# Performance work log

Measured on AMD Instinct MI355X. Metric: run time of the kernel, lower is better.

Reference implementation:

```python
import jax, jax.numpy as jnp
import numpy as np
import math

B, T, D, H, L, V = 2, 1024, 768, 12, 4, 50257
HD = D // H
ROPE_PCT = 0.5
MAX_WL = 10000.0
EPS = 1e-5


def setup_inputs() -> dict:
    key = jax.random.key(0)
    ks = jax.random.split(key, 8)
    s = 0.02
    return {
        "idx": jax.random.randint(ks[0], (B, T), 0, V, dtype=jnp.int32),
        "wte": jax.random.normal(ks[1], (V, D), jnp.float32) * s,
        "ln1_g": jnp.ones((L, D), jnp.float32),
        "ln1_b": jnp.zeros((L, D), jnp.float32),
        "Wqkv": jax.random.normal(ks[2], (L, D, 3 * D), jnp.float32) * s,
        "bqkv": jnp.zeros((L, 3 * D), jnp.float32),
        "Wo": jax.random.normal(ks[3], (L, D, D), jnp.float32) * s,
        "bo": jnp.zeros((L, D), jnp.float32),
        "ln2_g": jnp.ones((L, D), jnp.float32),
        "ln2_b": jnp.zeros((L, D), jnp.float32),
        "Wfc": jax.random.normal(ks[4], (L, D, 4 * D), jnp.float32) * s,
        "bfc": jnp.zeros((L, 4 * D), jnp.float32),
        "Wp": jax.random.normal(ks[5], (L, 4 * D, D), jnp.float32) * s,
        "bp": jnp.zeros((L, D), jnp.float32),
        "lnf_g": jnp.ones((D,), jnp.float32),
        "lnf_b": jnp.zeros((D,), jnp.float32),
        "Wlm": jax.random.normal(ks[6], (D, V), jnp.float32) * s,
    }


def _ln(x, g, b):
    m = x.mean(-1, keepdims=True)
    v = x.var(-1, keepdims=True)
    return (x - m) / jnp.sqrt(v + EPS) * g + b


def _gelu(x):
    return 0.5 * x * (1.0 + jnp.tanh(math.sqrt(2.0 / math.pi) * (x + 0.044715 * x ** 3)))


def _p_rope(x, positions):
    # x: [B, H, T, HD]; partial RoPE: rotate first ROPE_PCT of angle pairs, leave rest.
    rope_angles = int(ROPE_PCT * HD // 2)
    nope_angles = HD // 2 - rope_angles
    fraction = 2.0 * jnp.arange(0, rope_angles) / HD
    timescale = jnp.power(MAX_WL, fraction)
    timescale = jnp.pad(timescale, (0, nope_angles), constant_values=jnp.inf)
    sinusoid = positions[:, None] / timescale[None, :]  # [T, HD//2]; pos/inf = 0 -> no rotation
    sin, cos = jnp.sin(sinusoid), jnp.cos(sinusoid)
    first, second = jnp.split(x, 2, axis=-1)
    out = jnp.concatenate([first * cos - second * sin, second * cos + first * sin], axis=-1)
    return out.astype(x.dtype)


def reference(idx, wte, ln1_g, ln1_b, Wqkv, bqkv, Wo, bo, ln2_g, ln2_b, Wfc, bfc, Wp, bp, lnf_g, lnf_b, Wlm):
    x = wte[idx]  # [B, T, D]
    positions = jnp.arange(T, dtype=x.dtype)
    causal = jnp.tril(jnp.ones((T, T), dtype=bool))
    scale = jnp.sqrt(jnp.float32(HD)).astype(x.dtype)
    for l in range(L):
        h1 = _ln(x, ln1_g[l], ln1_b[l])
        h2 = _ln(x, ln2_g[l], ln2_b[l])  # note: both LNs read the same x (as in source)
        # attention
        qkv = h1 @ Wqkv[l] + bqkv[l]
        q, k, v = jnp.split(qkv, 3, axis=-1)
        sh = lambda t: t.reshape(B, T, H, HD).transpose(0, 2, 1, 3)
        q, k, v = sh(q), sh(k), sh(v)
        q = _p_rope(q, positions)
        k = _p_rope(k, positions)
        att = jnp.einsum('bhqd,bhkd->bhqk', q, k) / scale
        att = jnp.where(causal, att, jnp.finfo(att.dtype).min)
        att = jax.nn.softmax(att, axis=-1)
        y = jnp.einsum('bhqk,bhkd->bhqd', att, v)
        y = y.transpose(0, 2, 1, 3).reshape(B, T, D)
        x = x + (y @ Wo[l] + bo[l])
        # MLP
        h = _gelu(h2 @ Wfc[l] + bfc[l])
        x = x + (h @ Wp[l] + bp[l])
    x = _ln(x, lnf_g, lnf_b)
    logits = x @ Wlm  # [B, T, V]
    return logits
```

## Files before the change

### kernel.cpp

```cpp
#include <hip/hip_runtime.h>

typedef unsigned short u16;
typedef unsigned int u32;
typedef __attribute__((ext_vector_type(8))) short bf16x8;
typedef __attribute__((ext_vector_type(4))) float f32x4;

#define SEQ 1024
#define DM 768
#define NH 12
#define HD2 64
#define NLAYER 4
#define NVOCAB 50257
#define BT 2048

__device__ __forceinline__ u16 f2bf(float f) {
  union { float f; u32 u; } v; v.f = f;
  u32 r = v.u + 0x7FFFu + ((v.u >> 16) & 1u);
  return (u16)(r >> 16);
}
__device__ __forceinline__ float bf2f(u16 u) {
  union { u32 u; float f; } v; v.u = ((u32)u) << 16;
  return v.f;
}

__device__ __forceinline__ void glds16(const u16* g, u16* l) {
  __builtin_amdgcn_global_load_lds(
      (const __attribute__((address_space(1))) u32*)(const void*)g,
      (__attribute__((address_space(3))) u32*)(void*)l, 16, 0, 0);
}

__device__ __forceinline__ void cvt_tile(const float* __restrict__ in,
                                         u16* __restrict__ out, int R, int C,
                                         int cx, int ry, u16 (*t)[68]) {
  int c0 = cx * 64, r0 = ry * 64;
  int tx = threadIdx.x & 15, ty = threadIdx.x >> 4;
  int c = c0 + tx * 4;
#pragma unroll
  for (int i = 0; i < 4; ++i) {
    int r = r0 + ty + i * 16;
    float4 v = make_float4(0.f, 0.f, 0.f, 0.f);
    if (c + 3 < C) {
      v = *(const float4*)&in[(size_t)r * C + c];
    } else {
      if (c + 0 < C) v.x = in[(size_t)r * C + c];
      if (c + 1 < C) v.y = in[(size_t)r * C + c + 1];
      if (c + 2 < C) v.z = in[(size_t)r * C + c + 2];
      if (c + 3 < C) v.w = in[(size_t)r * C + c + 3];
    }
    t[ty + i * 16][tx * 4 + 0] = f2bf(v.x);
    t[ty + i * 16][tx * 4 + 1] = f2bf(v.y);
    t[ty + i * 16][tx * 4 + 2] = f2bf(v.z);
    t[ty + i * 16][tx * 4 + 3] = f2bf(v.w);
  }
  __syncthreads();
  int wl = threadIdx.x & 31, grp = threadIdx.x >> 5;
#pragma unroll
  for (int it = 0; it < 8; ++it) {
    int cc = it * 8 + grp;
    int gcol = c0 + cc;
    if (gcol < C) {
      u32 wv = (u32)t[2 * wl][cc] | ((u32)t[2 * wl + 1][cc] << 16);
      *(u32*)&out[(size_t)gcol * R + r0 + 2 * wl] = wv;
    }
  }
}

__global__ void k_prep(const int* __restrict__ idx, const float* __restrict__ wte,
                       float* __restrict__ xf, float* __restrict__ ctab,
                       float* __restrict__ stab, const float* __restrict__ Wqkv,
                       const float* __restrict__ Wo, const float* __restrict__ Wfc,
                       const float* __restrict__ Wp, const float* __restrict__ Wlm,
                       u16* __restrict__ wqkvT, u16* __restrict__ woT,
                       u16* __restrict__ wfcT, u16* __restrict__ wpT,
                       u16* __restrict__ wlmT) {
  __shared__ u16 t[64][68];
  int bid = blockIdx.x;
  if (bid < BT) {
    int tok = idx[bid];
    const float* s = wte + (size_t)tok * DM;
    float* d = xf + (size_t)bid * DM;
    for (int c = threadIdx.x; c < DM; c += 256) d[c] = s[c];
    return;
  }
  bid -= BT;
  if (bid < 64) {
    int gid = bid * 256 + threadIdx.x;
    int tt = gid >> 4, j = gid & 15;
    float inv = powf(10000.f, -(float)j * (1.f / 32.f));
    float ang = (float)tt * inv;
    ctab[gid] = cosf(ang);
    stab[gid] = sinf(ang);
    return;
  }
  bid -= 64;
  if (bid < NLAYER * 1728) {
    int layer = bid / 1728, r = bid % 1728;
    if (r < 432) {
      cvt_tile(Wqkv + (size_t)layer * DM * 3 * DM,
               wqkvT + (size_t)layer * 3 * DM * DM, DM, 3 * DM, r % 36, r / 36, t);
      return;
    }
    r -= 432;
    if (r < 144) {
      cvt_tile(Wo + (size_t)layer * DM * DM, woT + (size_t)layer * DM * DM,
               DM, DM, r % 12, r / 12, t);
      return;
    }
    r -= 144;
    if (r < 576) {
      cvt_tile(Wfc + (size_t)layer * DM * 4 * DM,
               wfcT + (size_t)layer * 4 * DM * DM, DM, 4 * DM, r % 48, r / 48, t);
      return;
    }
    r -= 576;
    cvt_tile(Wp + (size_t)layer * 4 * DM * DM, wpT + (size_t)layer * 4 * DM * DM,
             4 * DM, DM, r % 12, r / 12, t);
    return;
  }
  bid -= NLAYER * 1728;
  cvt_tile(Wlm, wlmT, DM, NVOCAB, bid % 786, bid / 786, t);
}

__global__ void k_ln(const float* __restrict__ x, const float* __restrict__ g1,
                     const float* __restrict__ b1, const float* __restrict__ g2,
                     const float* __restrict__ b2, u16* __restrict__ o1,
                     u16* __restrict__ o2) {
  int w = threadIdx.x >> 6, l = threadIdx.x & 63;
  int r = blockIdx.x * 4 + w;
  const float* xr = x + (size_t)r * DM;
  float2 v[6];
  float s = 0.f;
#pragma unroll
  for (int i = 0; i < 6; ++i) {
    v[i] = *(const float2*)&xr[2 * l + i * 128];
    s += v[i].x + v[i].y;
  }
#pragma unroll
  for (int o = 1; o < 64; o <<= 1) s += __shfl_xor(s, o);
  float mean = s * (1.f / DM);
  float vs = 0.f;
#pragma unroll
  for (int i = 0; i < 6; ++i) {
    float dx = v[i].x - mean, dy = v[i].y - mean;
    vs += dx * dx + dy * dy;
  }
#pragma unroll
  for (int o = 1; o < 64; o <<= 1) vs += __shfl_xor(vs, o);
  float rstd = rsqrtf(vs * (1.f / DM) + 1e-5f);
  u16* p1 = o1 + (size_t)r * DM;
#pragma unroll
  for (int i = 0; i < 6; ++i) {
    int c = 2 * l + i * 128;
    float2 gg = *(const float2*)&g1[c];
    float2 bb = *(const float2*)&b1[c];
    u32 wv = (u32)f2bf((v[i].x - mean) * rstd * gg.x + bb.x) |
             ((u32)f2bf((v[i].y - mean) * rstd * gg.y + bb.y) << 16);
    *(u32*)&p1[c] = wv;
  }
  if (o2) {
    u16* p2 = o2 + (size_t)r * DM;
#pragma unroll
    for (int i = 0; i < 6; ++i) {
      int c = 2 * l + i * 128;
      float2 gg = *(const float2*)&g2[c];
      float2 bb = *(const float2*)&b2[c];
      u32 wv = (u32)f2bf((v[i].x - mean) * rstd * gg.x + bb.x) |
               ((u32)f2bf((v[i].y - mean) * rstd * gg.y + bb.y) << 16);
      *(u32*)&p2[c] = wv;
    }
  }
}

__global__ void k_attn(const u16* __restrict__ qr, const u16* __restrict__ kr,
                       const u16* __restrict__ vT, u16* __restrict__ yb) {
  int ti = (int)gridDim.x - 1 - (int)blockIdx.x;
  int bh = blockIdx.y;
  __shared__ u16 Ps[64 * 72];
  __shared__ u16 Ks[2][4096];
  __shared__ u16 Vs[2][4096];
  int tid = threadIdx.x;
  int rr = tid >> 2, cc = tid & 3;
  int w = tid >> 6, l = tid & 63;
  int rl = l & 15, g = l >> 4;
  {
    const u16* gq = qr + ((size_t)bh * SEQ + ti * 64 + rr) * HD2;
    *(uint4*)&Ps[rr * 72 + cc * 8]      = *(const uint4*)(gq + cc * 8);
    *(uint4*)&Ps[rr * 72 + cc * 8 + 32] = *(const uint4*)(gq + cc * 8 + 32);
  }
  int srow = w * 8 + (l >> 3);
  int gs = (l & 7) ^ (l >> 3);
  const u16* gkb = kr + (size_t)bh * SEQ * HD2;
  const u16* gvb = vT + (size_t)bh * HD2 * SEQ;
  glds16(gkb + (size_t)srow * 64 + gs * 8,        &Ks[0][w * 512]);
  glds16(gkb + (size_t)(32 + srow) * 64 + gs * 8, &Ks[0][2048 + w * 512]);
  glds16(gvb + (size_t)srow * SEQ + gs * 8,       &Vs[0][w * 512]);
  glds16(gvb + (size_t)(32 + srow) * SEQ + gs * 8,&Vs[0][2048 + w * 512]);
  __syncthreads();
  bf16x8 aq0 = *(const bf16x8*)&Ps[(w * 16 + rl) * 72 + g * 8];
  bf16x8 aq1 = *(const bf16x8*)&Ps[(w * 16 + rl) * 72 + 32 + g * 8];
  float m[4], lsum[4];
  f32x4 oacc[4] = {};
#pragma unroll
  for (int r2 = 0; r2 < 4; ++r2) { m[r2] = -3.0e38f; lsum[r2] = 0.f; }
  int qloc = w * 16 + g * 4;
  int sw = rl & 7;
  int cur = 0;
  for (int kt = 0; kt <= ti; ++kt) {
    if (kt < ti) {
      int nx = cur ^ 1;
      glds16(gkb + (size_t)((kt + 1) * 64 + srow) * 64 + gs * 8,      &Ks[nx][w * 512]);
      glds16(gkb + (size_t)((kt + 1) * 64 + 32 + srow) * 64 + gs * 8, &Ks[nx][2048 + w * 512]);
      glds16(gvb + (size_t)srow * SEQ + (kt + 1) * 64 + gs * 8,       &Vs[nx][w * 512]);
      glds16(gvb + (size_t)(32 + srow) * SEQ + (kt + 1) * 64 + gs * 8,&Vs[nx][2048 + w * 512]);
    }
    f32x4 s[4] = {};
    __builtin_amdgcn_s_setprio(1);
#pragma unroll
    for (int nt = 0; nt < 4; ++nt) {
      int r = (nt * 16 + rl) * 64;
      bf16x8 b0 = *(const bf16x8*)&Ks[cur][r + ((0 + g) ^ sw) * 8];
      bf16x8 b1 = *(const bf16x8*)&Ks[cur][r + ((4 + g) ^ sw) * 8];
      s[nt] = __builtin_amdgcn_mfma_f32_16x16x32_bf16(aq0, b0, s[nt], 0, 0, 0);
      s[nt] = __builtin_amdgcn_mfma_f32_16x16x32_bf16(aq1, b1, s[nt], 0, 0, 0);
    }
    __builtin_amdgcn_s_setprio(0);
    if (kt == ti) {
#pragma unroll
      for (int nt = 0; nt < 4; ++nt) {
        int col = nt * 16 + rl;
#pragma unroll
        for (int r2 = 0; r2 < 4; ++r2)
          if (col > qloc + r2) s[nt][r2] = -3.0e38f;
      }
    }
#pragma unroll
    for (int r2 = 0; r2 < 4; ++r2) {
      float pm = fmaxf(fmaxf(s[0][r2], s[1][r2]), fmaxf(s[2][r2], s[3][r2]));
#pragma unroll
      for (int o = 1; o < 16; o <<= 1) pm = fmaxf(pm, __shfl_xor(pm, o));
      if (pm > m[r2] + 8.f) {
        float corr = __expf(m[r2] - pm);
        m[r2] = pm;
        lsum[r2] *= corr;
        oacc[0][r2] *= corr; oacc[1][r2] *= corr;
        oacc[2][r2] *= corr; oacc[3][r2] *= corr;
      }
      float p0 = __expf(s[0][r2] - m[r2]);
      float p1 = __expf(s[1][r2] - m[r2]);
      float p2 = __expf(s[2][r2] - m[r2]);
      float p3 = __expf(s[3][r2] - m[r2]);
      float ps = p0 + p1 + p2 + p3;
#pragma unroll
      for (int o = 1; o < 16; o <<= 1) ps += __shfl_xor(ps, o);
      lsum[r2] += ps;
      int prow = (qloc + r2) * 72;
      Ps[prow + rl]      = f2bf(p0);
      Ps[prow + 16 + rl] = f2bf(p1);
      Ps[prow + 32 + rl] = f2bf(p2);
      Ps[prow + 48 + rl] = f2bf(p3);
    }
    bf16x8 pa0 = *(const bf16x8*)&Ps[(w * 16 + rl) * 72 + g * 8];
    bf16x8 pa1 = *(const bf16x8*)&Ps[(w * 16 + rl) * 72 + 32 + g * 8];
    __builtin_amdgcn_s_setprio(1);
#pragma unroll
    for (int nt = 0; nt < 4; ++nt) {
      int r = (nt * 16 + rl) * 64;
      bf16x8 b0 = *(const bf16x8*)&Vs[cur][r + ((0 + g) ^ sw) * 8];
      bf16x8 b1 = *(const bf16x8*)&Vs[cur][r + ((4 + g) ^ sw) * 8];
      oacc[nt] = __builtin_amdgcn_mfma_f32_16x16x32_bf16(pa0, b0, oacc[nt], 0, 0, 0);
      oacc[nt] = __builtin_amdgcn_mfma_f32_16x16x32_bf16(pa1, b1, oacc[nt], 0, 0, 0);
    }
    __builtin_amdgcn_s_setprio(0);
    __syncthreads();
    cur ^= 1;
  }
  int b = bh / NH, h = bh % NH;
  float invl[4];
#pragma unroll
  for (int r2 = 0; r2 < 4; ++r2) invl[r2] = 1.f / lsum[r2];
#pragma unroll
  for (int nt = 0; nt < 4; ++nt) {
    int d = nt * 16 + rl;
#pragma unroll
    for (int r2 = 0; r2 < 4; ++r2) {
      int trow = ti * 64 + qloc + r2;
      yb[((size_t)(b * SEQ + trow)) * DM + h * HD2 + d] = f2bf(oacc[nt][r2] * invl[r2]);
    }
  }
}

template <int MODE>
__global__ void k_g128(const u16* __restrict__ A, const u16* __restrict__ Bt,
                       float* __restrict__ outf, int M, int N, int K, int MT) {
  __shared__ u16 SM[16384];
  float* cw = (float*)SM;
  int nwg = gridDim.x;
  int id = blockIdx.x;
  if ((nwg & 7) == 0) id = (id & 7) * (nwg >> 3) + (id >> 3);
  int mt = id % MT, nt = id / MT;
  int m0 = mt * 128, n0 = nt * 128;
  int tid = threadIdx.x;
  int w = tid >> 6, l = tid & 63;
  int srow = w * 16 + (l >> 2);
  int gs = (l & 3) ^ ((l >> 3) & 3);
  const u16* gA0 = A + (size_t)(m0 + srow) * K + gs * 8;
  const u16* gA1 = A + (size_t)(m0 + 64 + srow) * K + gs * 8;
  int rb0 = n0 + srow;      if (rb0 > N - 1) rb0 = N - 1;
  int rb1 = n0 + 64 + srow; if (rb1 > N - 1) rb1 = N - 1;
  const u16* gB0 = Bt + (size_t)rb0 * K + gs * 8;
  const u16* gB1 = Bt + (size_t)rb1 * K + gs * 8;
  int wm = (w >> 1) * 64, wn = (w & 1) * 64;
  int rl = l & 15, g = l >> 4;
  int sla = g ^ ((rl >> 1) & 3);
  f32x4 acc[4][4] = {};
  int nK = K >> 5;
  int cur = 0;
  {
    u16* dA = SM + w * 512;
    glds16(gA0, dA); glds16(gA1, dA + 2048);
    u16* dB = SM + 4096 + w * 512;
    glds16(gB0, dB); glds16(gB1, dB + 2048);
  }
  __syncthreads();
  for (int kt = 0; kt < nK; ++kt) {
    if (kt + 1 < nK) {
      u16* dA = SM + (cur ^ 1) * 8192 + w * 512;
      glds16(gA0 + (kt + 1) * 32, dA); glds16(gA1 + (kt + 1) * 32, dA + 2048);
      u16* dB = dA + 4096;
      glds16(gB0 + (kt + 1) * 32, dB); glds16(gB1 + (kt + 1) * 32, dB + 2048);
    }
    const u16* As = SM + cur * 8192;
    const u16* Bs = As + 4096;
    bf16x8 af[4], bfr[4];
    __builtin_amdgcn_s_setprio(1);
#pragma unroll
    for (int i = 0; i < 4; ++i)
      af[i] = *(const bf16x8*)&As[(wm + i * 16 + rl) * 32 + sla * 8];
#pragma unroll
    for (int j = 0; j < 4; ++j)
      bfr[j] = *(const bf16x8*)&Bs[(wn + j * 16 + rl) * 32 + sla * 8];
#pragma unroll
    for (int i = 0; i < 4; ++i)
#pragma unroll
      for (int j = 0; j < 4; ++j)
        acc[i][j] = __builtin_amdgcn_mfma_f32_16x16x32_bf16(af[i], bfr[j],
                                                            acc[i][j], 0, 0, 0);
    __builtin_amdgcn_s_setprio(0);
    __syncthreads();
    cur ^= 1;
  }
#pragma unroll
  for (int ch = 0; ch < 4; ++ch) {
    if ((w >> 1) == (ch >> 1)) {
      int ib = (ch & 1) * 2;
#pragma unroll
      for (int ii = 0; ii < 2; ++ii) {
#pragma unroll
        for (int j = 0; j < 4; ++j) {
          int col = wn + j * 16 + rl;
#pragma unroll
          for (int r2 = 0; r2 < 4; ++r2) {
            int rowc = ii * 16 + g * 4 + r2;
            cw[rowc * 132 + col] = acc[ib + ii][j][r2];
          }
        }
      }
    }
    __syncthreads();
    for (int t = tid; t < 4096; t += 256) {
      int rowc = t >> 7, col = t & 127;
      int gc = n0 + col;
      if (gc < N)
        __builtin_nontemporal_store(cw[rowc * 132 + col],
                                    &outf[(size_t)(m0 + ch * 32 + rowc) * N + gc]);
    }
    __syncthreads();
  }
}

template <int MODE>
__global__ void k_gw(const u16* __restrict__ A, const u16* __restrict__ Bt,
                     const float* __restrict__ bias, u16* __restrict__ outb,
                     int M, int N, int K, int MT,
                     const float* __restrict__ ctab,
                     const float* __restrict__ stab, u16* __restrict__ qrp,
                     u16* __restrict__ krp, u16* __restrict__ vTp) {
  __shared__ u16 SM2[24576];
  float* cw = (float*)SM2;
  int nwg = gridDim.x;
  int id = blockIdx.x;
  if ((nwg & 7) == 0) id = (id & 7) * (nwg >> 3) + (id >> 3);
  int mt = id % MT, nt = id / MT;
  int m0 = mt * 64, n0 = nt * 128;
  int tid = threadIdx.x;
  int w = tid >> 6, l = tid & 63;
  int row0 = tid >> 3, slot0 = tid & 7;
  int gs0 = slot0 ^ (row0 & 7);
  const u16* gA0 = A + (size_t)(m0 + row0) * K + gs0 * 8;
  const u16* gA1 = gA0 + (size_t)32 * K;
  const u16* gB0 = Bt + (size_t)(n0 + row0) * K + gs0 * 8;
  const u16* gB1 = gB0 + (size_t)32 * K;
  const u16* gB2 = gB0 + (size_t)64 * K;
  const u16* gB3 = gB0 + (size_t)96 * K;
  int wm = (w >> 1) * 32, wn = (w & 1) * 64;
  int rl = l & 15, g = l >> 4;
  int sl0 = g ^ (rl & 7), sl1 = (4 + g) ^ (rl & 7);
  f32x4 acc[2][4] = {};
  int nK = K >> 6;
  int cur = 0;
  {
    u16* dA = SM2;
    glds16(gA0, dA + w * 512); glds16(gA1, dA + 2048 + w * 512);
    u16* dB = SM2 + 8192;
    glds16(gB0, dB + w * 512);        glds16(gB1, dB + 2048 + w * 512);
    glds16(gB2, dB + 4096 + w * 512); glds16(gB3, dB + 6144 + w * 512);
  }
  __syncthreads();
  for (int kt = 0; kt < nK; ++kt) {
    if (kt + 1 < nK) {
      int ka = (kt + 1) * 64;
      u16* dA = SM2 + (cur ^ 1) * 4096;
      glds16(gA0 + ka, dA + w * 512); glds16(gA1 + ka, dA + 2048 + w * 512);
      u16* dB = SM2 + 8192 + (cur ^ 1) * 8192;
      glds16(gB0 + ka, dB + w * 512);        glds16(gB1 + ka, dB + 2048 + w * 512);
      glds16(gB2 + ka, dB + 4096 + w * 512); glds16(gB3 + ka, dB + 6144 + w * 512);
    }
    const u16* Ac = SM2 + cur * 4096;
    const u16* Bc = SM2 + 8192 + cur * 8192;
    bf16x8 a0[2], a1[2], b0[4], b1[4];
    __builtin_amdgcn_s_setprio(1);
#pragma unroll
    for (int i = 0; i < 2; ++i) {
      int r = (wm + i * 16 + rl) * 64;
      a0[i] = *(const bf16x8*)&Ac[r + sl0 * 8];
      a1[i] = *(const bf16x8*)&Ac[r + sl1 * 8];
    }
#pragma unroll
    for (int j = 0; j < 4; ++j) {
      int r = (wn + j * 16 + rl) * 64;
      b0[j] = *(const bf16x8*)&Bc[r + sl0 * 8];
      b1[j] = *(const bf16x8*)&Bc[r + sl1 * 8];
    }
#pragma unroll
    for (int i = 0; i < 2; ++i)
#pragma unroll
      for (int j = 0; j < 4; ++j) {
        acc[i][j] = __builtin_amdgcn_mfma_f32_16x16x32_bf16(a0[i], b0[j],
                                                            acc[i][j], 0, 0, 0);
        acc[i][j] = __builtin_amdgcn_mfma_f32_16x16x32_bf16(a1[i], b1[j],
                                                            acc[i][j], 0, 0, 0);
      }
    __builtin_amdgcn_s_setprio(0);
    __syncthreads();
    cur ^= 1;
  }
#pragma unroll
  for (int i = 0; i < 2; ++i) {
#pragma unroll
    for (int j = 0; j < 4; ++j) {
      int col = wn + j * 16 + rl;
      float bv = bias[n0 + col];
#pragma unroll
      for (int r2 = 0; r2 < 4; ++r2) {
        float v = acc[i][j][r2] + bv;
        if (MODE == 1) {
          float u = 0.7978845608028654f * (v + 0.044715f * v * v * v);
          v = 0.5f * v * (1.f + tanhf(u));
        }
        cw[(wm + i * 16 + g * 4 + r2) * 133 + col] = v;
      }
    }
  }
  __syncthreads();
  if (MODE == 1) {
    for (int t = tid; t < 4096; t += 256) {
      int rowc = t >> 6, cp = t & 63;
      u32 wv = (u32)f2bf(cw[rowc * 133 + 2 * cp]) |
               ((u32)f2bf(cw[rowc * 133 + 2 * cp + 1]) << 16);
      *(u32*)&outb[(size_t)(m0 + rowc) * N + n0 + 2 * cp] = wv;
    }
  } else {
    int reg = n0 / DM;
    int h0 = (n0 % DM) / 64;
    int bb = m0 >> 10;
    int t0 = m0 & (SEQ - 1);
    size_t bhb = (size_t)bb * NH + h0;
    if (reg < 2) {
      u16* dst = (reg == 0) ? qrp : krp;
      float qs = (reg == 0) ? 0.125f : 1.f;
      for (int t = tid; t < 4096; t += 256) {
        int rowc = t >> 6, cp = t & 63;
        int c = 2 * cp;
        int hh = c >> 6, d = c & 63;
        int tt = t0 + rowc;
        float x0 = cw[rowc * 133 + c];
        float x1 = cw[rowc * 133 + c + 1];
        float o0, o1;
        if (d < 32) {
          float y0 = cw[rowc * 133 + c + 32];
          float y1 = cw[rowc * 133 + c + 33];
          float c0 = 1.f, s0 = 0.f, c1 = 1.f, s1 = 0.f;
          if (d < 16) {
            c0 = ctab[tt * 16 + d];     s0 = stab[tt * 16 + d];
            c1 = ctab[tt * 16 + d + 1]; s1 = stab[tt * 16 + d + 1];
          }
          o0 = x0 * c0 - y0 * s0;
          o1 = x1 * c1 - y1 * s1;
        } else {
          int j = d - 32;
          float y0 = cw[rowc * 133 + c - 32];
          float y1 = cw[rowc * 133 + c - 31];
          float c0 = 1.f, s0 = 0.f, c1 = 1.f, s1 = 0.f;
          if (j < 16) {
            c0 = ctab[tt * 16 + j];     s0 = stab[tt * 16 + j];
            c1 = ctab[tt * 16 + j + 1]; s1 = stab[tt * 16 + j + 1];
          }
          o0 = x0 * c0 + y0 * s0;
          o1 = x1 * c1 + y1 * s1;
        }
        u32 wv = (u32)f2bf(o0 * qs) | ((u32)f2bf(o1 * qs) << 16);
        *(u32*)&dst[((bhb + hh) * SEQ + tt) * HD2 + d] = wv;
      }
    } else {
      for (int t = tid; t < 4096; t += 256) {
        int dcol = t >> 5, p = t & 31;
        int hh = dcol >> 6, d = dcol & 63;
        int tt = t0 + 2 * p;
        u32 wv = (u32)f2bf(cw[(2 * p) * 133 + dcol]) |
                 ((u32)f2bf(cw[(2 * p + 1) * 133 + dcol]) << 16);
        *(u32*)&vTp[((bhb + hh) * HD2 + d) * SEQ + tt] = wv;
      }
    }
  }
}

__global__ void k_g64r(const u16* __restrict__ A, const u16* __restrict__ Bt,
                       const float* __restrict__ bias,
                       float* __restrict__ outf, int M, int N, int K, int MT) {
  __shared__ u16 As[8192];
  __shared__ u16 Bs[8192];
  int nwg = gridDim.x;
  int id = blockIdx.x;
  if ((nwg & 7) == 0) id = (id & 7) * (nwg >> 3) + (id >> 3);
  int mt = id % MT, nt = id / MT;
  int sk = blockIdx.y, nsk = gridDim.y;
  int Kc = K / nsk, k0 = sk * Kc;
  int m0 = mt * 64, n0 = nt * 64;
  int tid = threadIdx.x;
  int w = tid >> 6, l = tid & 63;
  int row0 = tid >> 3, slot0 = tid & 7;
  int gs0 = slot0 ^ (row0 & 7);
  const u16* gA0 = A + (size_t)(m0 + row0) * K + k0 + gs0 * 8;
  const u16* gA1 = gA0 + (size_t)32 * K;
  const u16* gB0 = Bt + (size_t)(n0 + row0) * K + k0 + gs0 * 8;
  const u16* gB1 = gB0 + (size_t)32 * K;
  int wm = (w >> 1) * 32, wn = (w & 1) * 32;
  int rl = l & 15, g = l >> 4;
  int sl0 = g ^ (rl & 7), sl1 = (4 + g) ^ (rl & 7);
  f32x4 acc[2][2] = {};
  int nK = Kc >> 6;
  int cur = 0;
  {
    glds16(gA0, As + w * 512); glds16(gA1, As + 2048 + w * 512);
    glds16(gB0, Bs + w * 512); glds16(gB1, Bs + 2048 + w * 512);
  }
  __syncthreads();
  for (int kt = 0; kt < nK; ++kt) {
    if (kt + 1 < nK) {
      int nx = (cur ^ 1) * 4096;
      glds16(gA0 + (kt + 1) * 64, As + nx + w * 512);
      glds16(gA1 + (kt + 1) * 64, As + nx + 2048 + w * 512);
      glds16(gB0 + (kt + 1) * 64, Bs + nx + w * 512);
      glds16(gB1 + (kt + 1) * 64, Bs + nx + 2048 + w * 512);
    }
    const u16* Ac = As + cur * 4096;
    const u16* Bc = Bs + cur * 4096;
    bf16x8 a0[2], a1[2], b0[2], b1[2];
    __builtin_amdgcn_s_setprio(1);
#pragma unroll
    for (int i = 0; i < 2; ++i) {
      int r = (wm + i * 16 + rl) * 64;
      a0[i] = *(const bf16x8*)&Ac[r + sl0 * 8];
      a1[i] = *(const bf16x8*)&Ac[r + sl1 * 8];
    }
#pragma unroll
    for (int j = 0; j < 2; ++j) {
      int r = (wn + j * 16 + rl) * 64;
      b0[j] = *(const bf16x8*)&Bc[r + sl0 * 8];
      b1[j] = *(const bf16x8*)&Bc[r + sl1 * 8];
    }
#pragma unroll
    for (int i = 0; i < 2; ++i)
#pragma unroll
      for (int j = 0; j < 2; ++j) {
        acc[i][j] = __builtin_amdgcn_mfma_f32_16x16x32_bf16(a0[i], b0[j],
                                                            acc[i][j], 0, 0, 0);
        acc[i][j] = __builtin_amdgcn_mfma_f32_16x16x32_bf16(a1[i], b1[j],
                                                            acc[i][j], 0, 0, 0);
      }
    __builtin_amdgcn_s_setprio(0);
    __syncthreads();
    cur ^= 1;
  }
#pragma unroll
  for (int i = 0; i < 2; ++i) {
#pragma unroll
    for (int j = 0; j < 2; ++j) {
      int col = n0 + wn + j * 16 + rl;
      float bv = bias ? bias[col] : 0.f;
#pragma unroll
      for (int r2 = 0; r2 < 4; ++r2) {
        int row = m0 + wm + i * 16 + g * 4 + r2;
        float v = acc[i][j][r2];
        if (sk == 0) v += bv;
        atomicAdd(&outf[(size_t)row * N + col], v);
      }
    }
  }
}

__global__ void k_gemm_f32b(const u16* __restrict__ A, const float* __restrict__ B,
                            float* __restrict__ outf, int M, int N, int K) {
  __shared__ u16 As[128 * 40];
  __shared__ u16 Bs[4 * 128 * 12];
  int tid = threadIdx.x;
  int wid = tid >> 6, lane = tid & 63;
  int rl = lane & 15, g = lane >> 4;
  int m0 = blockIdx.x * 128, n0 = blockIdx.y * 128;
  int wm = (wid >> 1) * 64, wn = (wid & 1) * 64;
  int ar = tid >> 2, ac = tid & 3;
  int bn = tid & 127, bq = tid >> 7;
  f32x4 acc[4][4] = {};
  int nK = K / 32;
  for (int kt = 0; kt < nK; ++kt) {
    __syncthreads();
    {
      const u16* ga = A + (size_t)(m0 + ar) * K + kt * 32 + ac * 8;
      *(uint4*)&As[ar * 40 + ac * 8] = *(const uint4*)ga;
      *(uint4*)&As[(ar + 64) * 40 + ac * 8] = *(const uint4*)(ga + (size_t)64 * K);
    }
    int col = n0 + bn;
#pragma unroll
    for (int r = 0; r < 4; ++r) {
      int kq = bq + 2 * r;
      int kk = kt * 32 + kq * 4;
      float f0 = 0.f, f1 = 0.f, f2v = 0.f, f3 = 0.f;
      if (col < N) {
        const float* gb = B + (size_t)kk * N + col;
        f0 = gb[0]; f1 = gb[(size_t)N]; f2v = gb[(size_t)2 * N]; f3 = gb[(size_t)3 * N];
      }
      uint2 wv;
      wv.x = (u32)f2bf(f0) | ((u32)f2bf(f1) << 16);
      wv.y = (u32)f2bf(f2v) | ((u32)f2bf(f3) << 16);
      *(uint2*)&Bs[(kq >> 1) * 1536 + bn * 12 + (kq & 1) * 4] = wv;
    }
    __syncthreads();
    bf16x8 af[4], bfr[4];
#pragma unroll
    for (int mt = 0; mt < 4; ++mt)
      af[mt] = *(const bf16x8*)&As[(wm + mt * 16 + rl) * 40 + g * 8];
#pragma unroll
    for (int nt = 0; nt < 4; ++nt) {
      const u16* p = &Bs[g * 1536 + (wn + nt * 16 + rl) * 12];
      union { bf16x8 v; uint2 u2[2]; } tmp;
      tmp.u2[0] = *(const uint2*)p;
      tmp.u2[1] = *(const uint2*)(p + 4);
      bfr[nt] = tmp.v;
    }
#pragma unroll
    for (int mt = 0; mt < 4; ++mt)
#pragma unroll
      for (int nt = 0; nt < 4; ++nt)
        acc[mt][nt] = __builtin_amdgcn_mfma_f32_16x16x32_bf16(af[mt], bfr[nt],
                                                              acc[mt][nt], 0, 0, 0);
  }
#pragma unroll
  for (int mt = 0; mt < 4; ++mt)
#pragma unroll
    for (int nt = 0; nt < 4; ++nt) {
      int col = n0 + wn + nt * 16 + rl;
      if (col >= N) continue;
#pragma unroll
      for (int r2 = 0; r2 < 4; ++r2) {
        int row = m0 + wm + mt * 16 + g * 4 + r2;
        outf[(size_t)row * N + col] = acc[mt][nt][r2];
      }
    }
}

extern "C" void kernel_launch(void* const* d_in, const int* in_sizes, int n_in,
                              void* d_out, int out_size, void* d_ws, size_t ws_size,
                              hipStream_t stream) {
  (void)in_sizes; (void)n_in; (void)out_size;
  const int*   idx  = (const int*)  d_in[0];
  const float* wte  = (const float*)d_in[1];
  const float* ln1g = (const float*)d_in[2];
  const float* ln1b = (const float*)d_in[3];
  const float* Wqkv = (const float*)d_in[4];
  const float* bqkv = (const float*)d_in[5];
  const float* Wo   = (const float*)d_in[6];
  const float* bo   = (const float*)d_in[7];
  const float* ln2g = (const float*)d_in[8];
  const float* ln2b = (const float*)d_in[9];
  const float* Wfc  = (const float*)d_in[10];
  const float* bfc  = (const float*)d_in[11];
  const float* Wp   = (const float*)d_in[12];
  const float* bp   = (const float*)d_in[13];
  const float* lnfg = (const float*)d_in[14];
  const float* lnfb = (const float*)d_in[15];
  const float* Wlm  = (const float*)d_in[16];
  float* out = (float*)d_out;

  char* sb = (char*)d_out;
  size_t off = 0;
  auto alloc = [&](size_t bytes) {
    char* p = sb + off;
    off += (bytes + 255) & ~(size_t)255;
    return (void*)p;
  };
  float* xf  = (float*)alloc((size_t)BT * DM * 4);
  u16* h1b   = (u16*)alloc((size_t)BT * DM * 2);
  u16* h2b   = (u16*)alloc((size_t)BT * DM * 2);
  u16* qr    = (u16*)alloc((size_t)BT * DM * 2);
  u16* kr    = (u16*)alloc((size_t)BT * DM * 2);
  u16* vT    = (u16*)alloc((size_t)BT * DM * 2);
  u16* yb    = (u16*)alloc((size_t)BT * DM * 2);
  u16* hgel  = (u16*)alloc((size_t)BT * 4 * DM * 2);
  float* ctab = (float*)alloc((size_t)SEQ * 16 * 4);
  float* stab = (float*)alloc((size_t)SEQ * 16 * 4);
  u16* wqkvT = (u16*)alloc((size_t)NLAYER * 3 * DM * DM * 2);
  u16* woT   = (u16*)alloc((size_t)NLAYER * DM * DM * 2);
  u16* wfcT  = (u16*)alloc((size_t)NLAYER * 4 * DM * DM * 2);
  u16* wpT   = (u16*)alloc((size_t)NLAYER * 4 * DM * DM * 2);

  size_t wlmT_bytes = (size_t)NVOCAB * DM * 2;
  size_t xlnf_bytes = (size_t)BT * DM * 2;
  bool fast_lm = ws_size >= wlmT_bytes + xlnf_bytes + 512;
  u16* wlmT = (u16*)d_ws;
  u16* xlnf = fast_lm ? (u16*)((char*)d_ws + ((wlmT_bytes + 255) & ~(size_t)255))
                      : (u16*)d_ws;

  int prep_blocks = BT + 64 + NLAYER * 1728 + (fast_lm ? 9432 : 0);
  k_prep<<<prep_blocks, 256, 0, stream>>>(idx, wte, xf, ctab, stab,
                                          Wqkv, Wo, Wfc, Wp, Wlm,
                                          wqkvT, woT, wfcT, wpT, wlmT);

  for (int l = 0; l < NLAYER; ++l) {
    k_ln<<<BT / 4, 256, 0, stream>>>(xf, ln1g + l * DM, ln1b + l * DM,
                                     ln2g + l * DM, ln2b + l * DM, h1b, h2b);
    k_gw<4><<<(BT / 64) * (3 * DM / 128), 256, 0, stream>>>(
        h1b, wqkvT + (size_t)l * 3 * DM * DM, bqkv + (size_t)l * 3 * DM,
        nullptr, BT, 3 * DM, DM, BT / 64, ctab, stab, qr, kr, vT);
    k_attn<<<dim3(SEQ / 64, 2 * NH), 256, 0, stream>>>(qr, kr, vT, yb);
    k_g64r<<<dim3((BT / 64) * (DM / 64), 2), 256, 0, stream>>>(
        yb, woT + (size_t)l * DM * DM, bo + (size_t)l * DM, xf, BT, DM, DM, BT / 64);
    k_gw<1><<<(BT / 64) * (4 * DM / 128), 256, 0, stream>>>(
        h2b, wfcT + (size_t)l * 4 * DM * DM, bfc + (size_t)l * 4 * DM,
        hgel, BT, 4 * DM, DM, BT / 64, nullptr, nullptr, nullptr, nullptr, nullptr);
    k_g64r<<<dim3((BT / 64) * (DM / 64), 4), 256, 0, stream>>>(
        hgel, wpT + (size_t)l * 4 * DM * DM, bp + (size_t)l * DM, xf, BT, DM, 4 * DM,
        BT / 64);
  }
  k_ln<<<BT / 4, 256, 0, stream>>>(xf, lnfg, lnfb, nullptr, nullptr, xlnf, nullptr);
  if (fast_lm) {
    int nt = (NVOCAB + 127) / 128;
    k_g128<3><<<(BT / 128) * nt, 256, 0, stream>>>(
        xlnf, wlmT, out, BT, NVOCAB, DM, BT / 128);
  } else {
    k_gemm_f32b<<<dim3(BT / 128, (NVOCAB + 127) / 128), 256, 0, stream>>>(
        xlnf, Wlm, out, BT, NVOCAB, DM);
  }
}
```

Before: 898.0 us.

## Merge Wo projection and FC GEMM into one launch; skip softmax rescale per wave

The Wo split-K atomic GEMM and the FC+GELU GEMM are independent, so they are merged into a single kernel whose blocks branch by index: 768 FC tiles and 768 Wo split-K tiles. This removes one launch per layer and lets the two GEMMs fill the GPU together rather than run back to back. Separately, the attention online-softmax now computes local row maxima first and does the cross-lane shuffle reduction and rescale only when some lane in the wave needs a max update. The risks are uneven block work across the two branches, higher LDS use in the fused kernel, and extra branch overhead.

```diff
diff --git a/kernel.cpp b/kernel.cpp
--- a/kernel.cpp
+++ b/kernel.cpp
@@ -233,18 +233,29 @@
           if (col > qloc + r2) s[nt][r2] = -3.0e38f;
       }
     }
+    float lmax[4];
+#pragma unroll
+    for (int r2 = 0; r2 < 4; ++r2)
+      lmax[r2] = fmaxf(fmaxf(s[0][r2], s[1][r2]), fmaxf(s[2][r2], s[3][r2]));
+    bool need = (lmax[0] > m[0] + 8.f) || (lmax[1] > m[1] + 8.f) ||
+                (lmax[2] > m[2] + 8.f) || (lmax[3] > m[3] + 8.f);
+    if (__any(need)) {
+#pragma unroll
+      for (int r2 = 0; r2 < 4; ++r2) {
+        float pm = lmax[r2];
+#pragma unroll
+        for (int o = 1; o < 16; o <<= 1) pm = fmaxf(pm, __shfl_xor(pm, o));
+        if (pm > m[r2] + 8.f) {
+          float corr = __expf(m[r2] - pm);
+          m[r2] = pm;
+          lsum[r2] *= corr;
+          oacc[0][r2] *= corr; oacc[1][r2] *= corr;
+          oacc[2][r2] *= corr; oacc[3][r2] *= corr;
+        }
+      }
+    }
 #pragma unroll
     for (int r2 = 0; r2 < 4; ++r2) {
-      float pm = fmaxf(fmaxf(s[0][r2], s[1][r2]), fmaxf(s[2][r2], s[3][r2]));
-#pragma unroll
-      for (int o = 1; o < 16; o <<= 1) pm = fmaxf(pm, __shfl_xor(pm, o));
-      if (pm > m[r2] + 8.f) {
-        float corr = __expf(m[r2] - pm);
-        m[r2] = pm;
-        lsum[r2] *= corr;
-        oacc[0][r2] *= corr; oacc[1][r2] *= corr;
-        oacc[2][r2] *= corr; oacc[3][r2] *= corr;
-      }
       float p0 = __expf(s[0][r2] - m[r2]);
       float p1 = __expf(s[1][r2] - m[r2]);
       float p2 = __expf(s[2][r2] - m[r2]);
@@ -534,6 +545,182 @@
   }
 }
 
+__global__ void k_wofc(const u16* __restrict__ yb, const u16* __restrict__ woT,
+                       const float* __restrict__ bo, float* __restrict__ xf,
+                       const u16* __restrict__ h2b, const u16* __restrict__ wfcT,
+                       const float* __restrict__ bfc, u16* __restrict__ hgel) {
+  __shared__ u16 SM2[24576];
+  int nwg = gridDim.x;
+  int id = blockIdx.x;
+  id = (id & 7) * (nwg >> 3) + (id >> 3);
+  int tid = threadIdx.x;
+  int w = tid >> 6, l = tid & 63;
+  int rl = l & 15, g = l >> 4;
+  int row0 = tid >> 3, slot0 = tid & 7;
+  int gs0 = slot0 ^ (row0 & 7);
+  int sl0 = g ^ (rl & 7), sl1 = (4 + g) ^ (rl & 7);
+  if (id < 768) {
+    float* cw = (float*)SM2;
+    int mt = id % 32, nt = id / 32;
+    int m0 = mt * 64, n0 = nt * 128;
+    const int K = DM, N = 4 * DM;
+    const u16* gA0 = h2b + (size_t)(m0 + row0) * K + gs0 * 8;
+    const u16* gA1 = gA0 + (size_t)32 * K;
+    const u16* gB0 = wfcT + (size_t)(n0 + row0) * K + gs0 * 8;
+    const u16* gB1 = gB0 + (size_t)32 * K;
+    const u16* gB2 = gB0 + (size_t)64 * K;
+    const u16* gB3 = gB0 + (size_t)96 * K;
+    int wm = (w >> 1) * 32, wn = (w & 1) * 64;
+    f32x4 acc[2][4] = {};
+    int nK = K >> 6;
+    int cur = 0;
+    {
+      u16* dA = SM2;
+      glds16(gA0, dA + w * 512); glds16(gA1, dA + 2048 + w * 512);
+      u16* dB = SM2 + 8192;
+      glds16(gB0, dB + w * 512);        glds16(gB1, dB + 2048 + w * 512);
+      glds16(gB2, dB + 4096 + w * 512); glds16(gB3, dB + 6144 + w * 512);
+    }
+    __syncthreads();
+    for (int kt = 0; kt < nK; ++kt) {
+      if (kt + 1 < nK) {
+        int ka = (kt + 1) * 64;
+        u16* dA = SM2 + (cur ^ 1) * 4096;
+        glds16(gA0 + ka, dA + w * 512); glds16(gA1 + ka, dA + 2048 + w * 512);
+        u16* dB = SM2 + 8192 + (cur ^ 1) * 8192;
+        glds16(gB0 + ka, dB + w * 512);        glds16(gB1 + ka, dB + 2048 + w * 512);
+        glds16(gB2 + ka, dB + 4096 + w * 512); glds16(gB3 + ka, dB + 6144 + w * 512);
+      }
+      const u16* Ac = SM2 + cur * 4096;
+      const u16* Bc = SM2 + 8192 + cur * 8192;
+      bf16x8 a0[2], a1[2], b0[4], b1[4];
+      __builtin_amdgcn_s_setprio(1);
+#pragma unroll
+      for (int i = 0; i < 2; ++i) {
+        int r = (wm + i * 16 + rl) * 64;
+        a0[i] = *(const bf16x8*)&Ac[r + sl0 * 8];
+        a1[i] = *(const bf16x8*)&Ac[r + sl1 * 8];
+      }
+#pragma unroll
+      for (int j = 0; j < 4; ++j) {
+        int r = (wn + j * 16 + rl) * 64;
+        b0[j] = *(const bf16x8*)&Bc[r + sl0 * 8];
+        b1[j] = *(const bf16x8*)&Bc[r + sl1 * 8];
+      }
+#pragma unroll
+      for (int i = 0; i < 2; ++i)
+#pragma unroll
+        for (int j = 0; j < 4; ++j) {
+          acc[i][j] = __builtin_amdgcn_mfma_f32_16x16x32_bf16(a0[i], b0[j],
+                                                              acc[i][j], 0, 0, 0);
+          acc[i][j] = __builtin_amdgcn_mfma_f32_16x16x32_bf16(a1[i], b1[j],
+                                                              acc[i][j], 0, 0, 0);
+        }
+      __builtin_amdgcn_s_setprio(0);
+      __syncthreads();
+      cur ^= 1;
+    }
+#pragma unroll
+    for (int i = 0; i < 2; ++i) {
+#pragma unroll
+      for (int j = 0; j < 4; ++j) {
+        int col = wn + j * 16 + rl;
+        float bv = bfc[n0 + col];
+#pragma unroll
+        for (int r2 = 0; r2 < 4; ++r2) {
+          float v = acc[i][j][r2] + bv;
+          float u = 0.7978845608028654f * (v + 0.044715f * v * v * v);
+          v = 0.5f * v * (1.f + tanhf(u));
+          cw[(wm + i * 16 + g * 4 + r2) * 133 + col] = v;
+        }
+      }
+    }
+    __syncthreads();
+    for (int t = tid; t < 4096; t += 256) {
+      int rowc = t >> 6, cp = t & 63;
+      u32 wv = (u32)f2bf(cw[rowc * 133 + 2 * cp]) |
+               ((u32)f2bf(cw[rowc * 133 + 2 * cp + 1]) << 16);
+      *(u32*)&hgel[(size_t)(m0 + rowc) * N + n0 + 2 * cp] = wv;
+    }
+    return;
+  }
+  {
+    int id2 = id - 768;
+    int sk = id2 / 384, t = id2 % 384;
+    int mt = t % 32, nt = t / 32;
+    int m0 = mt * 64, n0 = nt * 64;
+    const int K = DM, N = DM;
+    int Kc = K / 2, k0 = sk * Kc;
+    u16* As = SM2;
+    u16* Bs = SM2 + 8192;
+    const u16* gA0 = yb + (size_t)(m0 + row0) * K + k0 + gs0 * 8;
+    const u16* gA1 = gA0 + (size_t)32 * K;
+    const u16* gB0 = woT + (size_t)(n0 + row0) * K + k0 + gs0 * 8;
+    const u16* gB1 = gB0 + (size_t)32 * K;
+    int wm = (w >> 1) * 32, wn = (w & 1) * 32;
+    f32x4 acc[2][2] = {};
+    int nK = Kc >> 6;
+    int cur = 0;
+    {
+      glds16(gA0, As + w * 512); glds16(gA1, As + 2048 + w * 512);
+      glds16(gB0, Bs + w * 512); glds16(gB1, Bs + 2048 + w * 512);
+    }
+    __syncthreads();
+    for (int kt = 0; kt < nK; ++kt) {
+      if (kt + 1 < nK) {
+        int nx = (cur ^ 1) * 4096;
+        glds16(gA0 + (kt + 1) * 64, As + nx + w * 512);
+        glds16(gA1 + (kt + 1) * 64, As + nx + 2048 + w * 512);
+        glds16(gB0 + (kt + 1) * 64, Bs + nx + w * 512);
+        glds16(gB1 + (kt + 1) * 64, Bs + nx + 2048 + w * 512);
+      }
+      const u16* Ac = As + cur * 4096;
+      const u16* Bc = Bs + cur * 4096;
+      bf16x8 a0[2], a1[2], b0[2], b1[2];
+      __builtin_amdgcn_s_setprio(1);
+#pragma unroll
+      for (int i = 0; i < 2; ++i) {
+        int r = (wm + i * 16 + rl) * 64;
+        a0[i] = *(const bf16x8*)&Ac[r + sl0 * 8];
+        a1[i] = *(const bf16x8*)&Ac[r + sl1 * 8];
+      }
+#pragma unroll
+      for (int j = 0; j < 2; ++j) {
+        int r = (wn + j * 16 + rl) * 64;
+        b0[j] = *(const bf16x8*)&Bc[r + sl0 * 8];
+        b1[j] = *(const bf16x8*)&Bc[r + sl1 * 8];
+      }
+#pragma unroll
+      for (int i = 0; i < 2; ++i)
+#pragma unroll
+        for (int j = 0; j < 2; ++j) {
+          acc[i][j] = __builtin_amdgcn_mfma_f32_16x16x32_bf16(a0[i], b0[j],
+                                                              acc[i][j], 0, 0, 0);
+          acc[i][j] = __builtin_amdgcn_mfma_f32_16x16x32_bf16(a1[i], b1[j],
+                                                              acc[i][j], 0, 0, 0);
+        }
+      __builtin_amdgcn_s_setprio(0);
+      __syncthreads();
+      cur ^= 1;
+    }
+#pragma unroll
+    for (int i = 0; i < 2; ++i) {
+#pragma unroll
+      for (int j = 0; j < 2; ++j) {
+        int col = n0 + wn + j * 16 + rl;
+        float bv = bo[col];
+#pragma unroll
+        for (int r2 = 0; r2 < 4; ++r2) {
+          int row = m0 + wm + i * 16 + g * 4 + r2;
+          float v = acc[i][j][r2];
+          if (sk == 0) v += bv;
+          atomicAdd(&xf[(size_t)row * N + col], v);
+        }
+      }
+    }
+  }
+}
+
 __global__ void k_g64r(const u16* __restrict__ A, const u16* __restrict__ Bt,
                        const float* __restrict__ bias,
                        float* __restrict__ outf, int M, int N, int K, int MT) {
@@ -752,11 +939,9 @@
         h1b, wqkvT + (size_t)l * 3 * DM * DM, bqkv + (size_t)l * 3 * DM,
         nullptr, BT, 3 * DM, DM, BT / 64, ctab, stab, qr, kr, vT);
     k_attn<<<dim3(SEQ / 64, 2 * NH), 256, 0, stream>>>(qr, kr, vT, yb);
-    k_g64r<<<dim3((BT / 64) * (DM / 64), 2), 256, 0, stream>>>(
-        yb, woT + (size_t)l * DM * DM, bo + (size_t)l * DM, xf, BT, DM, DM, BT / 64);
-    k_gw<1><<<(BT / 64) * (4 * DM / 128), 256, 0, stream>>>(
-        h2b, wfcT + (size_t)l * 4 * DM * DM, bfc + (size_t)l * 4 * DM,
-        hgel, BT, 4 * DM, DM, BT / 64, nullptr, nullptr, nullptr, nullptr, nullptr);
+    k_wofc<<<1536, 256, 0, stream>>>(
+        yb, woT + (size_t)l * DM * DM, bo + (size_t)l * DM, xf,
+        h2b, wfcT + (size_t)l * 4 * DM * DM, bfc + (size_t)l * 4 * DM, hgel);
     k_g64r<<<dim3((BT / 64) * (DM / 64), 4), 256, 0, stream>>>(
         hgel, wpT + (size_t)l * 4 * DM * DM, bp + (size_t)l * DM, xf, BT, DM, 4 * DM,
         BT / 64);
```

Result: faster. 876.8 us (median of 2 runs) (-2.4%).
